# Performance work log

Hardware: AMD Instinct MI355X
Metric: run time of the kernel (lower is better)

Reference implementation:

```python
import jax, jax.numpy as jnp
import numpy as np

B = 128          # batch (stands in for bit-packed words)
C, H, W = 3, 32, 32
K = 64           # num_kernels
RFS, STRIDE = 5, 1
HO = (H - RFS) // STRIDE + 1   # 28
P = HO * HO                     # 784 output positions
G0 = 8                          # 2**tree_depth, tree_depth=3
NL1, NL2, NCLS = 64000, 32000, 10

# ALL_OPERATIONS order; each gate is multilinear: c0 + ca*a + cb*b + cab*a*b
COEF = jnp.array([
    [0, 0, 0, 0],    # zero
    [0, 0, 0, 1],    # and
    [0, 1, 0, -1],   # not_implies (a & ~b)
    [0, 1, 0, 0],    # a
    [0, 0, 1, -1],   # not_implied_by (b & ~a)
    [0, 0, 1, 0],    # b
    [0, 1, 1, -2],   # xor
    [0, 1, 1, -1],   # or
    [1, -1, -1, 1],  # not_or
    [1, -1, -1, 2],  # not_xor
    [1, 0, -1, 0],   # not_b
    [1, 0, -1, 1],   # implied_by (~b | a)
    [1, -1, 0, 0],   # not_a
    [1, -1, 0, 1],   # implies (~a | b)
    [1, 0, 0, -1],   # not_and
    [1, 0, 0, 0],    # one
], dtype=jnp.float32)


def _gate(a, b, ops):
    # ops: int array broadcastable against a/b trailing dims
    c = COEF[ops]  # [..., 4]
    return c[..., 0] + c[..., 1] * a + c[..., 2] * b + c[..., 3] * (a * b)


def _forward(x, cl, cr, o0, o1, o2, o3, a1, b1, p1, a2, b2, p2):
    # Conv logic layer: gather level-0 operand pairs -> [B, K, P, G0]
    la = jnp.take(x, cl, axis=1)
    lb = jnp.take(x, cr, axis=1)
    g = _gate(la, lb, o0[:, None, :])            # ops per (kernel, gate)
    # Binary tree reduction: level l pairs gates (2i, 2i+1)
    for ops in (o1, o2, o3):
        g = _gate(g[..., 0::2], g[..., 1::2], ops[:, None, :])
    z = g[..., 0].reshape(x.shape[0], K * P)     # [B, 50176]
    # Logic linear layers: out[i] = gate(in[a[i]], in[b[i]], op[i])
    z = _gate(z[:, a1], z[:, b1], p1)            # [B, NL1]
    z = _gate(z[:, a2], z[:, b2], p2)            # [B, NL2]
    # GroupSum: popcount per class group
    return z.reshape(z.shape[0], NCLS, -1).sum(-1)  # [B, 10]


def setup_inputs() -> dict:
    key = jax.random.key(0)
    x = (jax.random.uniform(key, (B, C * H * W)) < 0.5).astype(jnp.float32)
    rng = np.random.default_rng(0)
    bh = np.repeat(np.arange(HO), HO)  # h_pos per position
    bw = np.tile(np.arange(HO), HO)    # w_pos per position

    def conv_idx():
        dh = rng.integers(0, RFS, (K, P, G0))
        dw = rng.integers(0, RFS, (K, P, G0))
        dc = rng.integers(0, C, (K, P, G0))
        idx = dc * H * W + (bh[None, :, None] * STRIDE + dh) * W + (bw[None, :, None] * STRIDE + dw)
        return jnp.asarray(idx.astype(np.int32))

    ops = lambda shape: jnp.asarray(rng.integers(0, 16, shape).astype(np.int32))
    ridx = lambda hi, n: jnp.asarray(rng.integers(0, hi, n).astype(np.int32))
    return {
        'x': x,
        'conv_left_idx': conv_idx(), 'conv_right_idx': conv_idx(),
        'conv_ops0': ops((K, G0)), 'conv_ops1': ops((K, 4)),
        'conv_ops2': ops((K, 2)), 'conv_ops3': ops((K, 1)),
        'lin1_a': ridx(K * P, NL1), 'lin1_b': ridx(K * P, NL1), 'lin1_ops': ops((NL1,)),
        'lin2_a': ridx(NL1, NL2), 'lin2_b': ridx(NL1, NL2), 'lin2_ops': ops((NL2,)),
    }


def reference(x, conv_left_idx, conv_right_idx, conv_ops0, conv_ops1, conv_ops2, conv_ops3,
              lin1_a, lin1_b, lin1_ops, lin2_a, lin2_b, lin2_ops):
    return _forward(x, conv_left_idx, conv_right_idx, conv_ops0, conv_ops1, conv_ops2, conv_ops3,
                    lin1_a, lin1_b, lin1_ops, lin2_a, lin2_b, lin2_ops)
```

## Files before the change

### kernel.cpp

```cpp
#include <hip/hip_runtime.h>
#include <stdint.h>

#define NFEAT 3072
#define NWORD 2
#define NK 64
#define NP 784
#define NG 8
#define KP (NK * NP)
#define NL1 64000
#define NL2 32000
#define NCLS 10
#define NB 128
#define JBLK 128

__device__ __forceinline__ uint64_t bsel64(uint64_t x, uint64_t p, uint64_t q) {
    return (x & p) | (~x & q);
}
__device__ __forceinline__ ulonglong2 gate128(ulonglong2 A, ulonglong2 B, int op) {
    uint64_t m3 = (uint64_t)0 - (uint64_t)((op >> 0) & 1);
    uint64_t m2 = (uint64_t)0 - (uint64_t)((op >> 1) & 1);
    uint64_t m1 = (uint64_t)0 - (uint64_t)((op >> 2) & 1);
    uint64_t m0 = (uint64_t)0 - (uint64_t)((op >> 3) & 1);
    ulonglong2 r;
    r.x = bsel64(A.x, bsel64(B.x, m3, m2), bsel64(B.x, m1, m0));
    r.y = bsel64(A.y, bsel64(B.y, m3, m2), bsel64(B.y, m1, m0));
    return r;
}

__global__ __launch_bounds__(256) void pack_kernel(const float* __restrict__ x,
                                                   uint64_t* __restrict__ xb,
                                                   float* __restrict__ out) {
    int gt = blockIdx.x * 256 + threadIdx.x;
    if (gt < NB * NCLS) out[gt] = 0.0f;
    int fw = gt >> 6;
    int lane = gt & 63;
    int f = fw >> 1, w = fw & 1;
    float val = x[(size_t)(w * 64 + lane) * NFEAT + f];
    uint64_t m = __ballot(val != 0.0f);
    if (lane == 0) xb[f * NWORD + w] = m;
}

__global__ __launch_bounds__(256) void conv_kernel(
    const uint64_t* __restrict__ xb,
    const int* __restrict__ cl, const int* __restrict__ cr,
    const int* __restrict__ o0, const int* __restrict__ o1,
    const int* __restrict__ o2, const int* __restrict__ o3,
    uint64_t* __restrict__ z) {
    __shared__ uint64_t sxb[NFEAT * NWORD];
    {
        ulonglong2* s2 = reinterpret_cast<ulonglong2*>(sxb);
        const ulonglong2* g2 = reinterpret_cast<const ulonglong2*>(xb);
        for (int i = threadIdx.x; i < NFEAT; i += blockDim.x)
            s2[i] = g2[i];
    }
    __syncthreads();

    int t = blockIdx.x * 256 + threadIdx.x;
    if (t >= KP) return;
    int k = t / NP;

    const int4* cl4 = reinterpret_cast<const int4*>(cl + (size_t)t * NG);
    const int4* cr4 = reinterpret_cast<const int4*>(cr + (size_t)t * NG);
    int4 l0 = cl4[0], l1 = cl4[1];
    int4 r0 = cr4[0], r1 = cr4[1];
    int la[NG] = {l0.x, l0.y, l0.z, l0.w, l1.x, l1.y, l1.z, l1.w};
    int rb[NG] = {r0.x, r0.y, r0.z, r0.w, r1.x, r1.y, r1.z, r1.w};

    int op0[NG], op1[4], op2[2], op3;
#pragma unroll
    for (int g = 0; g < NG; ++g) op0[g] = o0[k * NG + g];
#pragma unroll
    for (int g = 0; g < 4; ++g) op1[g] = o1[k * 4 + g];
#pragma unroll
    for (int g = 0; g < 2; ++g) op2[g] = o2[k * 2 + g];
    op3 = o3[k];

    const ulonglong2* sxb2 = reinterpret_cast<const ulonglong2*>(sxb);
    ulonglong2 gg[NG];
#pragma unroll
    for (int g = 0; g < NG; ++g) {
        ulonglong2 va = sxb2[la[g]];
        ulonglong2 vb = sxb2[rb[g]];
        gg[g] = gate128(va, vb, op0[g]);
    }
#pragma unroll
    for (int g = 0; g < 4; ++g)
        gg[g] = gate128(gg[2 * g], gg[2 * g + 1], op1[g]);
#pragma unroll
    for (int g = 0; g < 2; ++g)
        gg[g] = gate128(gg[2 * g], gg[2 * g + 1], op2[g]);
    reinterpret_cast<ulonglong2*>(z)[t] = gate128(gg[0], gg[1], op3);
}

__global__ __launch_bounds__(JBLK) void lin2_fused_kernel(
    const uint64_t* __restrict__ z,
    const int* __restrict__ a1, const int* __restrict__ b1,
    const int* __restrict__ p1,
    const int* __restrict__ a2, const int* __restrict__ b2,
    const int* __restrict__ p2, float* __restrict__ out) {
    __shared__ alignas(16) uint64_t s[NWORD][JBLK];
    int blk = blockIdx.x;
    const int chunks_per_cls = (NL2 / NCLS) / JBLK;
    int c = blk / chunks_per_cls;
    int j = c * (NL2 / NCLS) + (blk % chunks_per_cls) * JBLK + threadIdx.x;

    int ia = a2[j], ib = b2[j], op = p2[j];
    int iaa = a1[ia], iab = b1[ia], opa = p1[ia];
    int iba = a1[ib], ibb = b1[ib], opb = p1[ib];
    const ulonglong2* z2p = reinterpret_cast<const ulonglong2*>(z);
    ulonglong2 za = gate128(z2p[iaa], z2p[iab], opa);
    ulonglong2 zb = gate128(z2p[iba], z2p[ibb], opb);
    ulonglong2 zz = gate128(za, zb, op);
    s[0][threadIdx.x] = zz.x;
    s[1][threadIdx.x] = zz.y;
    __syncthreads();

    int bb = threadIdx.x;
    int w = bb >> 6, sh = bb & 63;
    const ulonglong2* sp = reinterpret_cast<const ulonglong2*>(s[w]);
    int cnt = 0;
#pragma unroll 16
    for (int jj = 0; jj < JBLK / 2; ++jj) {
        ulonglong2 v = sp[jj];
        cnt += (int)((v.x >> sh) & 1) + (int)((v.y >> sh) & 1);
    }
    atomicAdd(&out[bb * NCLS + c], (float)cnt);
}

extern "C" void kernel_launch(void* const* d_in, const int* in_sizes, int n_in,
                              void* d_out, int out_size, void* d_ws, size_t ws_size,
                              hipStream_t stream) {
    const float* x  = (const float*)d_in[0];
    const int* cl   = (const int*)d_in[1];
    const int* cr   = (const int*)d_in[2];
    const int* o0   = (const int*)d_in[3];
    const int* o1   = (const int*)d_in[4];
    const int* o2   = (const int*)d_in[5];
    const int* o3   = (const int*)d_in[6];
    const int* a1   = (const int*)d_in[7];
    const int* b1   = (const int*)d_in[8];
    const int* p1   = (const int*)d_in[9];
    const int* a2   = (const int*)d_in[10];
    const int* b2   = (const int*)d_in[11];
    const int* p2   = (const int*)d_in[12];
    float* out = (float*)d_out;

    uint8_t* ws = (uint8_t*)d_ws;
    uint64_t* xb = (uint64_t*)(ws);
    uint64_t* z  = (uint64_t*)(ws + 64 * 1024);

    pack_kernel<<<(NFEAT * NWORD * 64) / 256, 256, 0, stream>>>(x, xb, out);
    conv_kernel<<<(KP + 255) / 256, 256, 0, stream>>>(xb, cl, cr, o0, o1, o2, o3, z);
    lin2_fused_kernel<<<NL2 / JBLK, JBLK, 0, stream>>>(z, a1, b1, p1, a2, b2, p2, out);
}
```

Measured before the change: 96.77 us.

## Split fused lin1/lin2 work across two threads per output in lin2 kernel

Doubles the block size of the fused linear kernel so each lin2 output's two lin1 operand gates are computed by separate threads, exchanged through shared memory, then combined by the first 128 threads. The popcount loop is split between the two halves of the block, each doing half the words and issuing its own atomicAdd. This shortens the serial dependent gather chain per thread and raises memory-level parallelism, at the cost of an extra barrier, idle threads in the combine step, and twice as many atomics.

New measurement: 103.0 us. +6.4%, slower.

```diff
diff --git a/kernel.cpp b/kernel.cpp
--- a/kernel.cpp
+++ b/kernel.cpp
@@ -92,35 +92,42 @@
     reinterpret_cast<ulonglong2*>(z)[t] = gate128(gg[0], gg[1], op3);
 }
 
-__global__ __launch_bounds__(JBLK) void lin2_fused_kernel(
+__global__ __launch_bounds__(256) void lin2_fused_kernel(
     const uint64_t* __restrict__ z,
     const int* __restrict__ a1, const int* __restrict__ b1,
     const int* __restrict__ p1,
     const int* __restrict__ a2, const int* __restrict__ b2,
     const int* __restrict__ p2, float* __restrict__ out) {
-    __shared__ alignas(16) uint64_t s[NWORD][JBLK];
+    __shared__ alignas(16) ulonglong2 zs[256];
+    __shared__ alignas(16) uint64_t sbuf[NWORD * JBLK];
     int blk = blockIdx.x;
     const int chunks_per_cls = (NL2 / NCLS) / JBLK;
     int c = blk / chunks_per_cls;
-    int j = c * (NL2 / NCLS) + (blk % chunks_per_cls) * JBLK + threadIdx.x;
+    int jbase = c * (NL2 / NCLS) + (blk % chunks_per_cls) * JBLK;
 
-    int ia = a2[j], ib = b2[j], op = p2[j];
-    int iaa = a1[ia], iab = b1[ia], opa = p1[ia];
-    int iba = a1[ib], ibb = b1[ib], opb = p1[ib];
+    int u = threadIdx.x >> 1, role = threadIdx.x & 1;
+    int j = jbase + u;
+    int idx = role ? b2[j] : a2[j];
     const ulonglong2* z2p = reinterpret_cast<const ulonglong2*>(z);
-    ulonglong2 za = gate128(z2p[iaa], z2p[iab], opa);
-    ulonglong2 zb = gate128(z2p[iba], z2p[ibb], opb);
-    ulonglong2 zz = gate128(za, zb, op);
-    s[0][threadIdx.x] = zz.x;
-    s[1][threadIdx.x] = zz.y;
+    zs[threadIdx.x] = gate128(z2p[a1[idx]], z2p[b1[idx]], p1[idx]);
     __syncthreads();
 
-    int bb = threadIdx.x;
+    if (threadIdx.x < JBLK) {
+        ulonglong2 r = gate128(zs[2 * threadIdx.x], zs[2 * threadIdx.x + 1],
+                               p2[jbase + threadIdx.x]);
+        sbuf[threadIdx.x] = r.x;
+        sbuf[JBLK + threadIdx.x] = r.y;
+    }
+    __syncthreads();
+
+    int bb = threadIdx.x & 127;
+    int half = threadIdx.x >> 7;
     int w = bb >> 6, sh = bb & 63;
-    const ulonglong2* sp = reinterpret_cast<const ulonglong2*>(s[w]);
+    const ulonglong2* sp = reinterpret_cast<const ulonglong2*>(sbuf + w * JBLK)
+                           + half * (JBLK / 4);
     int cnt = 0;
-#pragma unroll 16
-    for (int jj = 0; jj < JBLK / 2; ++jj) {
+#pragma unroll
+    for (int jj = 0; jj < JBLK / 4; ++jj) {
         ulonglong2 v = sp[jj];
         cnt += (int)((v.x >> sh) & 1) + (int)((v.y >> sh) & 1);
     }
@@ -151,5 +158,5 @@
 
     pack_kernel<<<(NFEAT * NWORD * 64) / 256, 256, 0, stream>>>(x, xb, out);
     conv_kernel<<<(KP + 255) / 256, 256, 0, stream>>>(xb, cl, cr, o0, o1, o2, o3, z);
-    lin2_fused_kernel<<<NL2 / JBLK, JBLK, 0, stream>>>(z, a1, b1, p1, a2, b2, p2, out);
+    lin2_fused_kernel<<<NL2 / JBLK, 256, 0, stream>>>(z, a1, b1, p1, a2, b2, p2, out);
 }
```
